# Performance work log

Hardware: AMD Instinct MI355X
Metric: run time of the kernel (lower is better)

The kernel has to match this reference:

```python
import jax, jax.numpy as jnp
import numpy as np

B, C, T = 16, 256, 2048          # bsz, z_dim (fsz), tsz
PRED_STEPS, N_NEG, OFFSET = 12, 15, 16
COPIES = 1 + N_NEG


def setup_inputs() -> dict:
    key = jax.random.key(0)
    k1, k2, k3 = jax.random.split(key, 3)
    z = jax.random.normal(k1, (B, C, T), jnp.float32)
    # ConvTranspose2d(C, C, (1, PRED_STEPS)) weight, size-1 kernel-height dim dropped
    weight = jax.random.normal(k2, (C, C, PRED_STEPS), jnp.float32) * 0.02
    bias = jnp.zeros((C,), jnp.float32)
    # negative index sampling (done under no_grad in the original):
    # tszs[k] = k // N_NEG, r in [0, B*T-1), bump by 1 where r >= t
    tszs = jnp.repeat(jnp.arange(T, dtype=jnp.int32), N_NEG)   # (N_NEG*T,)
    r = jax.random.randint(k3, (B, N_NEG * T), 0, B * T - 1, dtype=jnp.int32)
    neg_idxs = r + (r >= tszs[None, :]).astype(jnp.int32)      # values in [0, B*T)
    return {"z": z, "weight": weight, "bias": bias, "neg_idxs": neg_idxs}


def reference(z, weight, bias, neg_idxs):
    # encoder / aggregator are identity: z_hat = z
    # predictor: pred_steps independent linear maps of z_hat
    z_pred = jnp.einsum('bct,coi->boti', z, weight) + bias[None, :, None, None]  # (B,C,T,S)

    # --- sample_negatives: gather from flattened (C, B*T) bank ---
    y = jnp.transpose(z, (1, 0, 2)).reshape(C, B * T)           # (C, B*T)
    negs = y[:, neg_idxs.reshape(-1)]                           # (C, B*N_NEG*T)
    negs = negs.reshape(C, B, N_NEG, T)
    negs = jnp.transpose(negs, (2, 1, 0, 3))                    # (N_NEG, B, C, T)

    targets = jnp.concatenate([z[None], negs], axis=0)          # (COPIES, B, C, T)

    steps = min(PRED_STEPS, T - OFFSET)
    preds = []
    for i in range(steps):  # fixed small structural loop (12 steps)
        off = i + OFFSET
        # ('bct,nbct->tbn') on the overlapping slices, written flat
        p = jnp.einsum('bct,nbct->tbn', z_pred[:, :, :T - off, i], targets[..., off:])
        preds.append(p.reshape(-1))
    predictions = jnp.concatenate(preds).reshape(-1, COPIES)
    labels = jnp.zeros((predictions.shape[0],), dtype=jnp.int32)
    return predictions, labels
```

## Files before the change

kernel.cpp:

```cpp
#include <hip/hip_runtime.h>
#include <hip/hip_bf16.h>

#define B_   16
#define C_   256
#define T_   2048
#define PS   12
#define NNEG 15
#define OFFS 16
#define COPIES 16

#define M_GEMM (B_ * T_)
#define N_GEMM (C_ * PS)
#define K_GEMM C_
#define NPRED 6225408
#define NLAB  389088

using bf16 = __hip_bfloat16;
typedef __attribute__((ext_vector_type(4))) float f32x4;
typedef __attribute__((ext_vector_type(8))) short bf16x8;

#define WAITVM(n) asm volatile("s_waitcnt vmcnt(" #n ")" ::: "memory")
#define GLL(src, dst)                                                        \
    __builtin_amdgcn_global_load_lds(                                        \
        (const __attribute__((address_space(1))) void*)(src),                \
        (__attribute__((address_space(3))) void*)(dst), 16, 0, 0)

__global__ __launch_bounds__(256) void transpose_z(const float* __restrict__ z,
                                                   bf16* __restrict__ zT) {
    __shared__ float tile[32][33];
    int t0 = blockIdx.x * 32, c0 = blockIdx.y * 32, b = blockIdx.z;
    int col = threadIdx.x & 31, r = threadIdx.x >> 5;
    for (int rr = 0; rr < 4; ++rr) {
        int row = r + rr * 8;
        tile[row][col] = z[(size_t)(b * C_ + c0 + row) * T_ + t0 + col];
    }
    __syncthreads();
    for (int rr = 0; rr < 4; ++rr) {
        int row = r + rr * 8;
        zT[(size_t)(b * T_ + t0 + row) * C_ + c0 + col] =
            __float2bfloat16(tile[col][row]);
    }
}

__global__ __launch_bounds__(256) void pack_w(const float* __restrict__ w,
                                              bf16* __restrict__ wTb) {
    int gid = blockIdx.x * 256 + threadIdx.x;
    int j = gid >> 8, c = gid & 255;
    int o = j & 255, i = j >> 8;
    wTb[gid] = __float2bfloat16(w[(size_t)c * (C_ * PS) + o * PS + i]);
}

#define EPAD 136

__global__ __launch_bounds__(256) void gemm_zpred(const bf16* __restrict__ zT,
                                                  const bf16* __restrict__ wTb,
                                                  const float* __restrict__ bias,
                                                  bf16* __restrict__ zp) {
    __shared__ __align__(16) char smem[49152];
    bf16* lE = (bf16*)smem;

    int bid = (blockIdx.x & 7) * 768 + (blockIdx.x >> 3);
    int bn = bid % (N_GEMM / 128);
    int bm = bid / (N_GEMM / 128);
    int tid = threadIdx.x;
    int wid = tid >> 6, lane = tid & 63;
    int ln15 = lane & 15, kg = lane >> 4;
    int wm = (wid & 1) * 64, wn = (wid >> 1) * 64;
    int row0 = bm * 128, col0 = bn * 128;
    int i_step = col0 >> 8;
    int o0 = col0 & 255;

    int gsw = ((lane & 3) ^ ((lane >> 3) & 3)) * 8;
    int srow = wid * 16 + (lane >> 2);
    const bf16* srcA = zT + (size_t)(row0 + srow) * 256 + gsw;
    const bf16* srcB = wTb + (size_t)(col0 + srow) * 256 + gsw;

    int offA[4], offB[4];
#pragma unroll
    for (int mi = 0; mi < 4; ++mi) {
        int r = wm + mi * 16 + ln15;
        offA[mi] = r * 64 + ((kg ^ ((r >> 1) & 3)) * 16);
    }
#pragma unroll
    for (int ni = 0; ni < 4; ++ni) {
        int c = wn + ni * 16 + ln15;
        offB[ni] = 8192 + c * 64 + ((kg ^ ((c >> 1) & 3)) * 16);
    }

    f32x4 acc[4][4] = {};

#define STAGE(t, slot_base)                                                  \
    {                                                                        \
        char* d = smem + (slot_base) + wid * 1024;                           \
        const bf16* sa = srcA + (t) * 32;                                    \
        const bf16* sb2 = srcB + (t) * 32;                                   \
        GLL(sa, d);                                                          \
        GLL(sa + 64 * 256, d + 4096);                                        \
        GLL(sb2, d + 8192);                                                  \
        GLL(sb2 + 64 * 256, d + 12288);                                      \
    }

#define TILE_BODY(slot_base, VMN)                                            \
    {                                                                        \
        WAITVM(VMN);                                                         \
        __builtin_amdgcn_s_barrier();                                        \
        const char* sb = smem + (slot_base);                                 \
        bf16x8 af[4], bfr[4];                                                \
        _Pragma("unroll") for (int mi = 0; mi < 4; ++mi)                     \
            af[mi] = *(const bf16x8*)(sb + offA[mi]);                        \
        _Pragma("unroll") for (int ni = 0; ni < 4; ++ni)                     \
            bfr[ni] = *(const bf16x8*)(sb + offB[ni]);                       \
        asm volatile("s_waitcnt lgkmcnt(0)" ::: "memory");                   \
        __builtin_amdgcn_sched_barrier(0);                                   \
        __builtin_amdgcn_s_barrier();                                        \
        __builtin_amdgcn_s_setprio(1);                                       \
        _Pragma("unroll") for (int mi = 0; mi < 4; ++mi)                     \
            _Pragma("unroll") for (int ni = 0; ni < 4; ++ni)                 \
                acc[mi][ni] = __builtin_amdgcn_mfma_f32_16x16x32_bf16(       \
                    af[mi], bfr[ni], acc[mi][ni], 0, 0, 0);                  \
        __builtin_amdgcn_s_setprio(0);                                       \
    }

    STAGE(0, 0);
    STAGE(1, 16384);
    STAGE(2, 32768);  TILE_BODY(0, 8);
    STAGE(3, 0);      TILE_BODY(16384, 8);
    STAGE(4, 16384);  TILE_BODY(32768, 8);
    STAGE(5, 32768);  TILE_BODY(0, 8);
    STAGE(6, 0);      TILE_BODY(16384, 8);
    STAGE(7, 16384);  TILE_BODY(32768, 8);
                      TILE_BODY(0, 4);
                      TILE_BODY(16384, 0);

    __syncthreads();

    float bv[4];
#pragma unroll
    for (int ni = 0; ni < 4; ++ni) bv[ni] = bias[o0 + wn + ni * 16 + ln15];

#pragma unroll
    for (int mi = 0; mi < 4; ++mi)
#pragma unroll
        for (int ni = 0; ni < 4; ++ni) {
            int col_e = wn + ni * 16 + ln15;
#pragma unroll
            for (int r = 0; r < 4; ++r) {
                int row_e = wm + mi * 16 + kg * 4 + r;
                lE[row_e * EPAD + col_e] = __float2bfloat16(acc[mi][ni][r] + bv[ni]);
            }
        }

    __syncthreads();

#pragma unroll
    for (int e = 0; e < 8; ++e) {
        int row_e = e * 16 + (tid >> 4);
        int grow = row0 + row_e;
        int b = grow >> 11, t = grow & (T_ - 1);
        int s = t + OFFS + i_step;
        if (s < T_) {
            bf16x8 v = *(const bf16x8*)&lE[row_e * EPAD + (tid & 15) * 8];
            *(bf16x8*)(zp + ((size_t)(b * T_ + s) * PS + i_step) * 256 + o0 +
                       (tid & 15) * 8) = v;
        }
    }
#undef STAGE
#undef TILE_BODY
}

__global__ __launch_bounds__(256) void predict_kernel(
    const bf16* __restrict__ zT, const bf16* __restrict__ zp,
    const int* __restrict__ neg, float* __restrict__ out) {
    __shared__ __align__(16) char psm[131072];
    int tid = threadIdx.x;
    int wid = tid >> 6, lane = tid & 63;
    int ln15 = lane & 15, kg = lane >> 4;
    char* my = psm + wid * 32768;
    int base_gi = (blockIdx.x * 4 + wid) * 8;

    const char* zTb = (const char*)zT;
    const char* zpb = (const char*)zp;

    auto stage = [&](int it, int slot) {
        int gi = base_gi + it;
        int b = gi / (T_ - OFFS);
        int s = OFFS + gi % (T_ - OFFS);
        int srcrow = 0;
        if (lane < 16) {
            if (lane == 0) srcrow = b * T_ + s;
            else srcrow = neg[b * (NNEG * T_) + (lane - 1) * T_ + s];
        }
        char* dst = my + slot * 16384;
        int half = lane >> 5;
        int g31 = lane & 31;
#pragma unroll
        for (int j = 0; j < 8; ++j) {
            int r0 = __shfl(srcrow, 2 * j);
            int r1 = __shfl(srcrow, 2 * j + 1);
            int row = half ? r1 : r0;
            int n = 2 * j + half;
            const char* src = zTb + (size_t)row * 512 + ((g31 ^ (n & 7)) << 4);
            GLL(src, dst + j * 1024);
        }
        size_t zoff = (size_t)(b * T_ + s) * (PS * 512);
#pragma unroll
        for (int j = 0; j < 6; ++j) {
            int i0 = 2 * j + half;
            const char* src = zpb + zoff + i0 * 512 + ((g31 ^ (i0 & 7)) << 4);
            GLL(src, dst + 8192 + j * 1024);
        }
    };

    auto compute = [&](int it, int slot) {
        const char* sb = my + slot * 16384;
        int ii = ln15 < 12 ? ln15 : 0;
        bf16x8 af[8], bfr[8];
#pragma unroll
        for (int kk = 0; kk < 8; ++kk) {
            int g = kk * 4 + kg;
            af[kk] = *(const bf16x8*)(sb + ln15 * 512 + ((g ^ (ln15 & 7)) << 4));
            bfr[kk] = *(const bf16x8*)(sb + 8192 + ii * 512 + ((g ^ (ii & 7)) << 4));
        }
        asm volatile("s_waitcnt lgkmcnt(0)" ::: "memory");
        __builtin_amdgcn_sched_barrier(0);
        if (it + 2 < 8) stage(it + 2, slot);

        f32x4 acc = {0.f, 0.f, 0.f, 0.f};
#pragma unroll
        for (int kk = 0; kk < 8; ++kk)
            acc = __builtin_amdgcn_mfma_f32_16x16x32_bf16(af[kk], bfr[kk], acc,
                                                          0, 0, 0);

        int gi = base_gi + it;
        int b = gi / (T_ - OFFS);
        int s = OFFS + gi % (T_ - OFFS);
        int i = ln15;
        int imax = s - OFFS; if (imax > PS - 1) imax = PS - 1;
        if (i <= imax) {
            int t = s - OFFS - i;
            int base_i = 256 * ((T_ - OFFS) * i - (i * (i - 1)) / 2);
            float* o = out + base_i + (t * B_ + b) * COPIES + kg * 4;
            o[0] = acc[0]; o[1] = acc[1]; o[2] = acc[2]; o[3] = acc[3];
        }
    };

    stage(0, 0);
    stage(1, 1);
#pragma unroll
    for (int it = 0; it < 8; ++it) {
        if (it < 7) { WAITVM(14); }
        else        { WAITVM(0);  }
        compute(it, it & 1);
    }
}

extern "C" void kernel_launch(void* const* d_in, const int* in_sizes, int n_in,
                              void* d_out, int out_size, void* d_ws, size_t ws_size,
                              hipStream_t stream) {
    const float* z    = (const float*)d_in[0];
    const float* w    = (const float*)d_in[1];
    const float* bias = (const float*)d_in[2];
    const int*   neg  = (const int*)d_in[3];
    float* out = (float*)d_out;

    char* ws = (char*)d_ws;
    const size_t ZP_BYTES = (size_t)B_ * T_ * PS * 256 * sizeof(bf16);
    bf16* zp  = (bf16*)ws;
    bf16* zT  = (bf16*)(ws + ZP_BYTES + 8192);
    bf16* wTb = (bf16*)(ws + ZP_BYTES + 8192 + (size_t)M_GEMM * 256 * sizeof(bf16));

    transpose_z<<<dim3(T_ / 32, C_ / 32, B_), 256, 0, stream>>>(z, zT);
    pack_w<<<(N_GEMM * 256) / 256, 256, 0, stream>>>(w, wTb);
    gemm_zpred<<<(M_GEMM / 128) * (N_GEMM / 128), 256, 0, stream>>>(zT, wTb, bias, zp);
    predict_kernel<<<(B_ * (T_ - OFFS)) / 32, 256, 0, stream>>>(zT, zp, neg, out);
    hipMemsetAsync(out + NPRED, 0, NLAB * sizeof(float), stream);
}
```

Measured before the change: 152.0 us.

## Split GEMM and predict kernels into batch slices to keep zp cache-resident

Processes the batch in two slices of eight, running the z_pred GEMM and then the predict kernel per slice on a smaller zp buffer. The intermediate zp buffer shrinks by half, so it is more likely to stay in the last-level cache between producer and consumer instead of going through HBM. In exchange it adds two more kernel launches and smaller grids, which means more tail and launch overhead.

```diff
diff --git a/kernel.cpp b/kernel.cpp
--- a/kernel.cpp
+++ b/kernel.cpp
@@ -14,6 +14,9 @@
 #define K_GEMM C_
 #define NPRED 6225408
 #define NLAB  389088
+
+#define BSLICE 8
+#define NSLICE (B_ / BSLICE)
 
 using bf16 = __hip_bfloat16;
 typedef __attribute__((ext_vector_type(4))) float f32x4;
@@ -55,18 +58,20 @@
 __global__ __launch_bounds__(256) void gemm_zpred(const bf16* __restrict__ zT,
                                                   const bf16* __restrict__ wTb,
                                                   const float* __restrict__ bias,
-                                                  bf16* __restrict__ zp) {
+                                                  bf16* __restrict__ zp,
+                                                  int b_base) {
     __shared__ __align__(16) char smem[49152];
     bf16* lE = (bf16*)smem;
 
-    int bid = (blockIdx.x & 7) * 768 + (blockIdx.x >> 3);
+    int bid = (blockIdx.x & 7) * 384 + (blockIdx.x >> 3);
     int bn = bid % (N_GEMM / 128);
     int bm = bid / (N_GEMM / 128);
     int tid = threadIdx.x;
     int wid = tid >> 6, lane = tid & 63;
     int ln15 = lane & 15, kg = lane >> 4;
     int wm = (wid & 1) * 64, wn = (wid >> 1) * 64;
-    int row0 = bm * 128, col0 = bn * 128;
+    int row0 = b_base * T_ + bm * 128;
+    int col0 = bn * 128;
     int i_step = col0 >> 8;
     int o0 = col0 & 255;
 
@@ -156,11 +161,12 @@
     for (int e = 0; e < 8; ++e) {
         int row_e = e * 16 + (tid >> 4);
         int grow = row0 + row_e;
-        int b = grow >> 11, t = grow & (T_ - 1);
+        int bl = (grow >> 11) - b_base;
+        int t = grow & (T_ - 1);
         int s = t + OFFS + i_step;
         if (s < T_) {
             bf16x8 v = *(const bf16x8*)&lE[row_e * EPAD + (tid & 15) * 8];
-            *(bf16x8*)(zp + ((size_t)(b * T_ + s) * PS + i_step) * 256 + o0 +
+            *(bf16x8*)(zp + ((size_t)(bl * T_ + s) * PS + i_step) * 256 + o0 +
                        (tid & 15) * 8) = v;
         }
     }
@@ -170,7 +176,7 @@
 
 __global__ __launch_bounds__(256) void predict_kernel(
     const bf16* __restrict__ zT, const bf16* __restrict__ zp,
-    const int* __restrict__ neg, float* __restrict__ out) {
+    const int* __restrict__ neg, float* __restrict__ out, int b_base) {
     __shared__ __align__(16) char psm[131072];
     int tid = threadIdx.x;
     int wid = tid >> 6, lane = tid & 63;
@@ -183,7 +189,8 @@
 
     auto stage = [&](int it, int slot) {
         int gi = base_gi + it;
-        int b = gi / (T_ - OFFS);
+        int bl = gi / (T_ - OFFS);
+        int b = b_base + bl;
         int s = OFFS + gi % (T_ - OFFS);
         int srcrow = 0;
         if (lane < 16) {
@@ -202,7 +209,7 @@
             const char* src = zTb + (size_t)row * 512 + ((g31 ^ (n & 7)) << 4);
             GLL(src, dst + j * 1024);
         }
-        size_t zoff = (size_t)(b * T_ + s) * (PS * 512);
+        size_t zoff = (size_t)(bl * T_ + s) * (PS * 512);
 #pragma unroll
         for (int j = 0; j < 6; ++j) {
             int i0 = 2 * j + half;
@@ -232,7 +239,7 @@
                                                           0, 0, 0);
 
         int gi = base_gi + it;
-        int b = gi / (T_ - OFFS);
+        int b = b_base + gi / (T_ - OFFS);
         int s = OFFS + gi % (T_ - OFFS);
         int i = ln15;
         int imax = s - OFFS; if (imax > PS - 1) imax = PS - 1;
@@ -264,14 +271,22 @@
     float* out = (float*)d_out;
 
     char* ws = (char*)d_ws;
-    const size_t ZP_BYTES = (size_t)B_ * T_ * PS * 256 * sizeof(bf16);
+    const size_t ZP_SLICE_BYTES =
+        (size_t)BSLICE * T_ * PS * 256 * sizeof(bf16);
     bf16* zp  = (bf16*)ws;
-    bf16* zT  = (bf16*)(ws + ZP_BYTES + 8192);
-    bf16* wTb = (bf16*)(ws + ZP_BYTES + 8192 + (size_t)M_GEMM * 256 * sizeof(bf16));
+    bf16* zT  = (bf16*)(ws + ZP_SLICE_BYTES + 8192);
+    bf16* wTb = (bf16*)(ws + ZP_SLICE_BYTES + 8192 +
+                        (size_t)M_GEMM * 256 * sizeof(bf16));
 
     transpose_z<<<dim3(T_ / 32, C_ / 32, B_), 256, 0, stream>>>(z, zT);
     pack_w<<<(N_GEMM * 256) / 256, 256, 0, stream>>>(w, wTb);
-    gemm_zpred<<<(M_GEMM / 128) * (N_GEMM / 128), 256, 0, stream>>>(zT, wTb, bias, zp);
-    predict_kernel<<<(B_ * (T_ - OFFS)) / 32, 256, 0, stream>>>(zT, zp, neg, out);
+
+    for (int sl = 0; sl < NSLICE; ++sl) {
+        int b_base = sl * BSLICE;
+        gemm_zpred<<<(BSLICE * T_ / 128) * (N_GEMM / 128), 256, 0, stream>>>(
+            zT, wTb, bias, zp, b_base);
+        predict_kernel<<<(BSLICE * (T_ - OFFS)) / 32, 256, 0, stream>>>(
+            zT, zp, neg, out, b_base);
+    }
     hipMemsetAsync(out + NPRED, 0, NLAB * sizeof(float), stream);
 }
```

Result: slower. 159.8 us (+5.1%).
